# Optimization experiments

Hardware: AMD Instinct MI355X
Metric: run time of the kernel (lower is better)

## Reference

```python
import jax, jax.numpy as jnp
import numpy as np

B, S, D, H, L, C = 64, 2048, 64, 256, 2, 8  # batch, seq, input, hidden, layers, classes


def setup_inputs() -> dict:
    key = jax.random.key(0)
    ks = jax.random.split(key, 12)
    k = 1.0 / np.sqrt(H)  # torch LSTM/Linear init scale
    u = lambda kk, shape: jax.random.uniform(kk, shape, jnp.float32, -k, k)
    x = jax.random.normal(ks[0], (B, S, D), jnp.float32)
    lengths = jax.random.randint(ks[1], (B,), 1, S + 1).astype(jnp.int32)
    return {
        "x": x,
        "lengths": lengths,
        "Wih0": u(ks[2], (4 * H, D)),
        "Whh0": u(ks[3], (4 * H, H)),
        "bih0": u(ks[4], (4 * H,)),
        "bhh0": u(ks[5], (4 * H,)),
        "Wih1": u(ks[6], (4 * H, H)),
        "Whh1": u(ks[7], (4 * H, H)),
        "bih1": u(ks[8], (4 * H,)),
        "bhh1": u(ks[9], (4 * H,)),
        "Wfc": u(ks[10], (C, H)),
        "bfc": u(ks[11], (C,)),
    }


def _lstm_layer(x, Wih, Whh, bih, bhh):
    # x: [B,S,Din] -> h-sequence [B,S,H]; torch gate order i,f,g,o
    pre = jnp.einsum('bsd,gd->bsg', x, Wih) + bih + bhh  # [B,S,4H]
    Hh = Whh.shape[1]
    bsz = x.shape[0]

    def step(carry, p_t):
        h, c = carry
        gates = p_t + h @ Whh.T  # [B,4H]
        i, f, g, o = jnp.split(gates, 4, axis=-1)
        i = jax.nn.sigmoid(i)
        f = jax.nn.sigmoid(f)
        g = jnp.tanh(g)
        o = jax.nn.sigmoid(o)
        c = f * c + i * g
        h = o * jnp.tanh(c)
        return (h, c), h

    init = (jnp.zeros((bsz, Hh), x.dtype), jnp.zeros((bsz, Hh), x.dtype))
    _, hs = jax.lax.scan(step, init, jnp.swapaxes(pre, 0, 1))  # [S,B,H]
    return jnp.swapaxes(hs, 0, 1)


def reference(x, lengths, Wih0, Whh0, bih0, bhh0, Wih1, Whh1, bih1, bhh1, Wfc, bfc):
    h1 = _lstm_layer(x, Wih0, Whh0, bih0, bhh0)   # [B,S,H]
    h2 = _lstm_layer(h1, Wih1, Whh1, bih1, bhh1)  # [B,S,H]
    # pad_packed_sequence zeros outputs beyond each sequence's length
    valid = (jnp.arange(S)[None, :] < lengths[:, None])[..., None]  # [B,S,1]
    h2 = jnp.where(valid, h2, 0.0)
    emissions = jnp.einsum('bsh,ch->bsc', h2, Wfc) + bfc  # [B,S,C]
    return emissions
```

## Files before the change

kernel.cpp:

```cpp
#include <hip/hip_runtime.h>
#include <hip/hip_bf16.h>

#define BATCH 64
#define SEQ   2048
#define DIN   64
#define HID   256
#define G4H   1024
#define NCLS  8

__device__ __forceinline__ float sigm(float x)  { return 1.0f / (1.0f + __expf(-x)); }
__device__ __forceinline__ float tanh_f(float x){ return 1.0f - 2.0f / (__expf(2.0f * x) + 1.0f); }

__global__ void init_out_kernel(float* __restrict__ out, const float* __restrict__ bfc) {
    int idx = blockIdx.x * blockDim.x + threadIdx.x;
    if (idx < BATCH * SEQ * NCLS) out[idx] = bfc[idx & 7];
}

__global__ __launch_bounds__(1024) void lstm_l0_kernel(
    const float* __restrict__ x,    const float* __restrict__ Wih0,
    const float* __restrict__ Whh0, const float* __restrict__ bih0,
    const float* __restrict__ bhh0, float* __restrict__ hist,
    const float* __restrict__ h1s_in, float* __restrict__ h1s_out,
    float* __restrict__ c1s, int* __restrict__ flagsA, int t0, int t1)
{
    const int bx  = blockIdx.x;
    const int b   = bx & 63;
    const int mem = bx >> 6;
    const int tid = threadIdx.x;
    const int p   = tid >> 8;
    const int r   = tid & 255;
    const int row = (r >> 6) * 256 + mem * 64 + (r & 63);

    float w[80];
#pragma unroll
    for (int q = 0; q < 80; ++q) {
        int col = p * 80 + q;
        w[q] = (col < DIN) ? Wih0[row * DIN + col] : Whh0[row * HID + (col - DIN)];
    }
    float biasv = 0.f;
    if (tid < 256) {
        int row2 = (tid >> 6) * 256 + mem * 64 + (tid & 63);
        biasv = bih0[row2] + bhh0[row2];
    }
    float creg = 0.f;
    if (tid < 64) creg = c1s[b * HID + mem * 64 + tid];

    __shared__ __align__(16) float v[320];
    __shared__ float pbuf[1024];
    __shared__ float act[256];

    for (int t = t0; t < t1; ++t) {
        if (t > t0 && tid < 4) {
            while (__hip_atomic_load(&flagsA[b * 4 + tid], __ATOMIC_ACQUIRE,
                                     __HIP_MEMORY_SCOPE_AGENT) < t) {}
        }
        __syncthreads();
        if (tid < 64) {
            v[tid] = x[((size_t)b * SEQ + t) * DIN + tid];
        } else if (tid < 320) {
            int j = tid - 64;
            v[tid] = (t == t0)
                ? h1s_in[b * HID + j]
                : __hip_atomic_load(&hist[((size_t)(t - 1 - t0) * BATCH + b) * HID + j],
                                    __ATOMIC_RELAXED, __HIP_MEMORY_SCOPE_AGENT);
        }
        __syncthreads();

        float a0 = 0.f, a1 = 0.f, a2 = 0.f, a3 = 0.f;
#pragma unroll
        for (int qq = 0; qq < 20; ++qq) {
            float4 vv = *(const float4*)&v[p * 80 + qq * 4];
            a0 = fmaf(w[qq * 4 + 0], vv.x, a0);
            a1 = fmaf(w[qq * 4 + 1], vv.y, a1);
            a2 = fmaf(w[qq * 4 + 2], vv.z, a2);
            a3 = fmaf(w[qq * 4 + 3], vv.w, a3);
        }
        pbuf[tid] = (a0 + a1) + (a2 + a3);
        __syncthreads();

        if (tid < 256) {
            float s = pbuf[tid] + pbuf[256 + tid] + pbuf[512 + tid] + pbuf[768 + tid] + biasv;
            act[tid] = ((tid >> 6) == 2) ? tanh_f(s) : sigm(s);
        }
        __syncthreads();

        if (tid < 64) {
            float iv = act[tid], fv = act[64 + tid], gv = act[128 + tid], ov = act[192 + tid];
            creg = fv * creg + iv * gv;
            float h = ov * tanh_f(creg);
            __hip_atomic_store(&hist[((size_t)(t - t0) * BATCH + b) * HID + mem * 64 + tid],
                               h, __ATOMIC_RELAXED, __HIP_MEMORY_SCOPE_AGENT);
            if (t == t1 - 1) {
                h1s_out[b * HID + mem * 64 + tid] = h;
                c1s[b * HID + mem * 64 + tid]     = creg;
            }
        }
        __syncthreads();
        if (tid == 0) {
            __hip_atomic_store(&flagsA[b * 4 + mem], t + 1, __ATOMIC_RELEASE,
                               __HIP_MEMORY_SCOPE_AGENT);
        }
    }
}

__global__ __launch_bounds__(1024) void lstm_l1_kernel(
    const float* __restrict__ hist, const float* __restrict__ Wih1,
    const float* __restrict__ Whh1, const float* __restrict__ bih1,
    const float* __restrict__ bhh1, const float* __restrict__ Wfc,
    const int* __restrict__ lengths, float* __restrict__ out,
    const float* __restrict__ h2s_in, float* __restrict__ h2s_out,
    float* __restrict__ c2s, float* __restrict__ xbuf,
    int* __restrict__ flagsB, int t0, int t1)
{
    const int bx  = blockIdx.x;
    const int bp  = bx & 31;
    const int mem = bx >> 5;
    const int tid = threadIdx.x;
    const int p   = tid >> 7;
    const int r   = tid & 127;
    const int row = (r >> 5) * 256 + mem * 32 + (r & 31);

    float w[64];
#pragma unroll
    for (int q = 0; q < 64; ++q) {
        int col = p * 64 + q;
        w[q] = (col < HID) ? Wih1[row * HID + col] : Whh1[row * HID + (col - HID)];
    }
    float biasv = 0.f;
    if (tid < 256) {
        int rr = tid & 127;
        int row2 = (rr >> 5) * 256 + mem * 32 + (rr & 31);
        biasv = bih1[row2] + bhh1[row2];
    }
    float creg = 0.f;
    if (tid < 64) {
        int n = tid >> 5, j2 = tid & 31;
        creg = c2s[(bp * 2 + n) * HID + mem * 32 + j2];
    }
    float wfc_r = 0.f; int mylen = 0;
    if (tid < 512) {
        int n = tid >> 8, c = (tid >> 5) & 7, j3 = tid & 31;
        wfc_r = Wfc[c * HID + mem * 32 + j3];
        mylen = lengths[bp * 2 + n];
    }

    __shared__ __align__(16) float vbuf[1024];
    __shared__ float pbuf[2048];
    __shared__ float act[256];
    __shared__ float hloc[64];

    for (int t = t0; t < t1; ++t) {
        if (t > t0 && tid < 8) {
            while (__hip_atomic_load(&flagsB[bp * 8 + tid], __ATOMIC_ACQUIRE,
                                     __HIP_MEMORY_SCOPE_AGENT) < t) {}
        }
        __syncthreads();
        if (tid < 512) {
            int n = tid >> 8, j = tid & 255;
            float hv = (t == t0)
                ? h2s_in[(bp * 2 + n) * HID + j]
                : __hip_atomic_load(&xbuf[((bp * 2 + n) * 2 + ((t - 1) & 1)) * HID + j],
                                    __ATOMIC_RELAXED, __HIP_MEMORY_SCOPE_AGENT);
            vbuf[n * 512 + HID + j] = hv;
        } else {
            int k = tid - 512;
            int n = k >> 8, j = k & 255;
            vbuf[n * 512 + j] = hist[((size_t)(t - t0) * BATCH + (bp * 2 + n)) * HID + j];
        }
        __syncthreads();

        float acc0 = 0.f, acc1 = 0.f;
#pragma unroll
        for (int qq = 0; qq < 16; ++qq) {
            float4 va = *(const float4*)&vbuf[p * 64 + qq * 4];
            acc0 = fmaf(w[qq * 4 + 0], va.x, acc0);
            acc0 = fmaf(w[qq * 4 + 1], va.y, acc0);
            acc0 = fmaf(w[qq * 4 + 2], va.z, acc0);
            acc0 = fmaf(w[qq * 4 + 3], va.w, acc0);
            float4 vb = *(const float4*)&vbuf[512 + p * 64 + qq * 4];
            acc1 = fmaf(w[qq * 4 + 0], vb.x, acc1);
            acc1 = fmaf(w[qq * 4 + 1], vb.y, acc1);
            acc1 = fmaf(w[qq * 4 + 2], vb.z, acc1);
            acc1 = fmaf(w[qq * 4 + 3], vb.w, acc1);
        }
        pbuf[p * 128 + r]        = acc0;
        pbuf[1024 + p * 128 + r] = acc1;
        __syncthreads();

        if (tid < 256) {
            int n = tid >> 7, rr = tid & 127;
            float s = biasv;
#pragma unroll
            for (int q = 0; q < 8; ++q) s += pbuf[n * 1024 + q * 128 + rr];
            act[n * 128 + rr] = ((rr >> 5) == 2) ? tanh_f(s) : sigm(s);
        }
        __syncthreads();

        if (tid < 64) {
            int n = tid >> 5, j2 = tid & 31;
            float iv = act[n * 128 + j2],      fv = act[n * 128 + 32 + j2];
            float gv = act[n * 128 + 64 + j2], ov = act[n * 128 + 96 + j2];
            creg = fv * creg + iv * gv;
            float h = ov * tanh_f(creg);
            hloc[tid] = h;
            __hip_atomic_store(&xbuf[((bp * 2 + n) * 2 + (t & 1)) * HID + mem * 32 + j2],
                               h, __ATOMIC_RELAXED, __HIP_MEMORY_SCOPE_AGENT);
            if (t == t1 - 1) {
                h2s_out[(bp * 2 + n) * HID + mem * 32 + j2] = h;
                c2s[(bp * 2 + n) * HID + mem * 32 + j2]     = creg;
            }
        }
        __syncthreads();
        if (tid == 0) {
            __hip_atomic_store(&flagsB[bp * 8 + mem], t + 1, __ATOMIC_RELEASE,
                               __HIP_MEMORY_SCOPE_AGENT);
        }
        if (tid < 512) {
            int n = tid >> 8, c = (tid >> 5) & 7, j3 = tid & 31;
            float val = (t < mylen) ? hloc[n * 32 + j3] * wfc_r : 0.f;
            val += __shfl_xor(val, 1);
            val += __shfl_xor(val, 2);
            val += __shfl_xor(val, 4);
            val += __shfl_xor(val, 8);
            val += __shfl_xor(val, 16);
            if (j3 == 0)
                atomicAdd(&out[((size_t)(bp * 2 + n) * SEQ + t) * NCLS + c], val);
        }
    }
}

extern "C" void kernel_launch(void* const* d_in, const int* in_sizes, int n_in,
                              void* d_out, int out_size, void* d_ws, size_t ws_size,
                              hipStream_t stream) {
    (void)in_sizes; (void)n_in; (void)out_size;
    const float* x     = (const float*)d_in[0];
    const int*   lens  = (const int*)  d_in[1];
    const float* Wih0  = (const float*)d_in[2];
    const float* Whh0  = (const float*)d_in[3];
    const float* bih0  = (const float*)d_in[4];
    const float* bhh0  = (const float*)d_in[5];
    const float* Wih1  = (const float*)d_in[6];
    const float* Whh1  = (const float*)d_in[7];
    const float* bih1  = (const float*)d_in[8];
    const float* bhh1  = (const float*)d_in[9];
    const float* Wfc   = (const float*)d_in[10];
    const float* bfc   = (const float*)d_in[11];
    float* out = (float*)d_out;
    char*  ws  = (char*)d_ws;

    int*   flagsA = (int*)(ws + 0);
    int*   flagsB = (int*)(ws + 1024);
    float* h1sA   = (float*)(ws + 2048);
    float* h1sB   = (float*)(ws + 2048 + 1 * 65536);
    float* c1s    = (float*)(ws + 2048 + 2 * 65536);
    float* h2sA   = (float*)(ws + 2048 + 3 * 65536);
    float* h2sB   = (float*)(ws + 2048 + 4 * 65536);
    float* c2s    = (float*)(ws + 2048 + 5 * 65536);
    float* xbuf   = (float*)(ws + 2048 + 6 * 65536);
    size_t hist_off = 2048 + 6 * 65536 + 131072;
    hist_off = (hist_off + 255) & ~(size_t)255;
    float* hist = (float*)(ws + hist_off);

    const size_t step_bytes = (size_t)BATCH * HID * 4;
    if (ws_size < hist_off + step_bytes) return;
    long avail = (long)(ws_size - hist_off);
    int Tc = (int)(avail / (long)step_bytes);
    if (Tc > SEQ) Tc = SEQ;
    if (Tc < 1)  Tc = 1;

    hipMemsetAsync(ws, 0, hist_off, stream);
    init_out_kernel<<<(BATCH * SEQ * NCLS + 255) / 256, 256, 0, stream>>>(out, bfc);

    int flip = 0;
    for (int t0 = 0; t0 < SEQ; t0 += Tc) {
        int t1 = t0 + Tc; if (t1 > SEQ) t1 = SEQ;
        float* h1in  = flip ? h1sB : h1sA;
        float* h1out = flip ? h1sA : h1sB;
        float* h2in  = flip ? h2sB : h2sA;
        float* h2out = flip ? h2sA : h2sB;
        lstm_l0_kernel<<<256, 1024, 0, stream>>>(x, Wih0, Whh0, bih0, bhh0, hist,
                                                 h1in, h1out, c1s, flagsA, t0, t1);
        lstm_l1_kernel<<<256, 1024, 0, stream>>>(hist, Wih1, Whh1, bih1, bhh1, Wfc,
                                                 lens, out, h2in, h2out, c2s, xbuf,
                                                 flagsB, t0, t1);
        flip ^= 1;
    }
}
```

Measured before the change: 19.92 ms.

## Regroup LSTM work per block and run whole sequence in single launches

Layer 0 now has each block handle two batch rows and a 32-unit slice, so the 256-block grid uses 8 member blocks per batch pair. Layer 1 has each block handle four batch rows and a 16-unit slice, with 16-way flag synchronisation. The output projection is now computed from the previous step's hidden state inside the step's existing barriers and stored directly instead of through atomicAdd. Time chunking is removed and a full-sequence history buffer is required, which drops the saved h/c state between chunks but needs a larger workspace. The layer-1 loop also removes one barrier per step, and the sync groups get wider, which may raise spin-wait cost.

```diff
diff --git a/kernel.cpp b/kernel.cpp
--- a/kernel.cpp
+++ b/kernel.cpp
@@ -5,7 +5,6 @@
 #define SEQ   2048
 #define DIN   64
 #define HID   256
-#define G4H   1024
 #define NCLS  8
 
 __device__ __forceinline__ float sigm(float x)  { return 1.0f / (1.0f + __expf(-x)); }
@@ -16,175 +15,79 @@
     if (idx < BATCH * SEQ * NCLS) out[idx] = bfc[idx & 7];
 }
 
-__global__ __launch_bounds__(1024) void lstm_l0_kernel(
+__global__ void lstm_l0_kernel(
     const float* __restrict__ x,    const float* __restrict__ Wih0,
     const float* __restrict__ Whh0, const float* __restrict__ bih0,
     const float* __restrict__ bhh0, float* __restrict__ hist,
-    const float* __restrict__ h1s_in, float* __restrict__ h1s_out,
-    float* __restrict__ c1s, int* __restrict__ flagsA, int t0, int t1)
+    int* __restrict__ flagsA)
 {
-    const int bx  = blockIdx.x;
-    const int b   = bx & 63;
-    const int mem = bx >> 6;
-    const int tid = threadIdx.x;
-    const int p   = tid >> 8;
-    const int r   = tid & 255;
-    const int row = (r >> 6) * 256 + mem * 64 + (r & 63);
-
-    float w[80];
-#pragma unroll
-    for (int q = 0; q < 80; ++q) {
-        int col = p * 80 + q;
-        w[q] = (col < DIN) ? Wih0[row * DIN + col] : Whh0[row * HID + (col - DIN)];
-    }
-    float biasv = 0.f;
-    if (tid < 256) {
-        int row2 = (tid >> 6) * 256 + mem * 64 + (tid & 63);
-        biasv = bih0[row2] + bhh0[row2];
-    }
-    float creg = 0.f;
-    if (tid < 64) creg = c1s[b * HID + mem * 64 + tid];
-
-    __shared__ __align__(16) float v[320];
-    __shared__ float pbuf[1024];
-    __shared__ float act[256];
-
-    for (int t = t0; t < t1; ++t) {
-        if (t > t0 && tid < 4) {
-            while (__hip_atomic_load(&flagsA[b * 4 + tid], __ATOMIC_ACQUIRE,
-                                     __HIP_MEMORY_SCOPE_AGENT) < t) {}
-        }
-        __syncthreads();
-        if (tid < 64) {
-            v[tid] = x[((size_t)b * SEQ + t) * DIN + tid];
-        } else if (tid < 320) {
-            int j = tid - 64;
-            v[tid] = (t == t0)
-                ? h1s_in[b * HID + j]
-                : __hip_atomic_load(&hist[((size_t)(t - 1 - t0) * BATCH + b) * HID + j],
-                                    __ATOMIC_RELAXED, __HIP_MEMORY_SCOPE_AGENT);
-        }
-        __syncthreads();
-
-        float a0 = 0.f, a1 = 0.f, a2 = 0.f, a3 = 0.f;
-#pragma unroll
-        for (int qq = 0; qq < 20; ++qq) {
-            float4 vv = *(const float4*)&v[p * 80 + qq * 4];
-            a0 = fmaf(w[qq * 4 + 0], vv.x, a0);
-            a1 = fmaf(w[qq * 4 + 1], vv.y, a1);
-            a2 = fmaf(w[qq * 4 + 2], vv.z, a2);
-            a3 = fmaf(w[qq * 4 + 3], vv.w, a3);
-        }
-        pbuf[tid] = (a0 + a1) + (a2 + a3);
-        __syncthreads();
-
-        if (tid < 256) {
-            float s = pbuf[tid] + pbuf[256 + tid] + pbuf[512 + tid] + pbuf[768 + tid] + biasv;
-            act[tid] = ((tid >> 6) == 2) ? tanh_f(s) : sigm(s);
-        }
-        __syncthreads();
-
-        if (tid < 64) {
-            float iv = act[tid], fv = act[64 + tid], gv = act[128 + tid], ov = act[192 + tid];
-            creg = fv * creg + iv * gv;
-            float h = ov * tanh_f(creg);
-            __hip_atomic_store(&hist[((size_t)(t - t0) * BATCH + b) * HID + mem * 64 + tid],
-                               h, __ATOMIC_RELAXED, __HIP_MEMORY_SCOPE_AGENT);
-            if (t == t1 - 1) {
-                h1s_out[b * HID + mem * 64 + tid] = h;
-                c1s[b * HID + mem * 64 + tid]     = creg;
-            }
-        }
-        __syncthreads();
-        if (tid == 0) {
-            __hip_atomic_store(&flagsA[b * 4 + mem], t + 1, __ATOMIC_RELEASE,
-                               __HIP_MEMORY_SCOPE_AGENT);
-        }
-    }
-}
-
-__global__ __launch_bounds__(1024) void lstm_l1_kernel(
-    const float* __restrict__ hist, const float* __restrict__ Wih1,
-    const float* __restrict__ Whh1, const float* __restrict__ bih1,
-    const float* __restrict__ bhh1, const float* __restrict__ Wfc,
-    const int* __restrict__ lengths, float* __restrict__ out,
-    const float* __restrict__ h2s_in, float* __restrict__ h2s_out,
-    float* __restrict__ c2s, float* __restrict__ xbuf,
-    int* __restrict__ flagsB, int t0, int t1)
-{
-    const int bx  = blockIdx.x;
-    const int bp  = bx & 31;
-    const int mem = bx >> 5;
+    const int P   = blockIdx.x & 31;
+    const int mem = blockIdx.x >> 5;
     const int tid = threadIdx.x;
     const int p   = tid >> 7;
     const int r   = tid & 127;
     const int row = (r >> 5) * 256 + mem * 32 + (r & 31);
 
-    float w[64];
-#pragma unroll
-    for (int q = 0; q < 64; ++q) {
-        int col = p * 64 + q;
-        w[q] = (col < HID) ? Wih1[row * HID + col] : Whh1[row * HID + (col - HID)];
-    }
+    float w[40];
+#pragma unroll
+    for (int q = 0; q < 40; ++q) {
+        int col = p * 40 + q;
+        w[q] = (col < DIN) ? Wih0[row * DIN + col] : Whh0[row * HID + (col - DIN)];
+    }
+#pragma unroll
+    for (int q = 0; q < 40; ++q) asm volatile("" : "+v"(w[q]));
+
     float biasv = 0.f;
     if (tid < 256) {
         int rr = tid & 127;
         int row2 = (rr >> 5) * 256 + mem * 32 + (rr & 31);
-        biasv = bih1[row2] + bhh1[row2];
-    }
+        biasv = bih0[row2] + bhh0[row2];
+    }
+    asm volatile("" : "+v"(biasv));
     float creg = 0.f;
-    if (tid < 64) {
-        int n = tid >> 5, j2 = tid & 31;
-        creg = c2s[(bp * 2 + n) * HID + mem * 32 + j2];
-    }
-    float wfc_r = 0.f; int mylen = 0;
-    if (tid < 512) {
-        int n = tid >> 8, c = (tid >> 5) & 7, j3 = tid & 31;
-        wfc_r = Wfc[c * HID + mem * 32 + j3];
-        mylen = lengths[bp * 2 + n];
-    }
-
-    __shared__ __align__(16) float vbuf[1024];
+
+    __shared__ __align__(16) float v[640];
     __shared__ float pbuf[2048];
     __shared__ float act[256];
-    __shared__ float hloc[64];
-
-    for (int t = t0; t < t1; ++t) {
-        if (t > t0 && tid < 8) {
-            while (__hip_atomic_load(&flagsB[bp * 8 + tid], __ATOMIC_ACQUIRE,
+
+    for (int t = 0; t < SEQ; ++t) {
+        if (t > 0 && tid < 8) {
+            while (__hip_atomic_load(&flagsA[P * 8 + tid], __ATOMIC_ACQUIRE,
                                      __HIP_MEMORY_SCOPE_AGENT) < t) {}
         }
         __syncthreads();
-        if (tid < 512) {
-            int n = tid >> 8, j = tid & 255;
-            float hv = (t == t0)
-                ? h2s_in[(bp * 2 + n) * HID + j]
-                : __hip_atomic_load(&xbuf[((bp * 2 + n) * 2 + ((t - 1) & 1)) * HID + j],
-                                    __ATOMIC_RELAXED, __HIP_MEMORY_SCOPE_AGENT);
-            vbuf[n * 512 + HID + j] = hv;
-        } else {
-            int k = tid - 512;
-            int n = k >> 8, j = k & 255;
-            vbuf[n * 512 + j] = hist[((size_t)(t - t0) * BATCH + (bp * 2 + n)) * HID + j];
-        }
-        __syncthreads();
-
-        float acc0 = 0.f, acc1 = 0.f;
-#pragma unroll
-        for (int qq = 0; qq < 16; ++qq) {
-            float4 va = *(const float4*)&vbuf[p * 64 + qq * 4];
-            acc0 = fmaf(w[qq * 4 + 0], va.x, acc0);
-            acc0 = fmaf(w[qq * 4 + 1], va.y, acc0);
-            acc0 = fmaf(w[qq * 4 + 2], va.z, acc0);
-            acc0 = fmaf(w[qq * 4 + 3], va.w, acc0);
-            float4 vb = *(const float4*)&vbuf[512 + p * 64 + qq * 4];
-            acc1 = fmaf(w[qq * 4 + 0], vb.x, acc1);
-            acc1 = fmaf(w[qq * 4 + 1], vb.y, acc1);
-            acc1 = fmaf(w[qq * 4 + 2], vb.z, acc1);
-            acc1 = fmaf(w[qq * 4 + 3], vb.w, acc1);
-        }
-        pbuf[p * 128 + r]        = acc0;
-        pbuf[1024 + p * 128 + r] = acc1;
+        if (tid < 640) {
+            int n = (tid >= 320) ? 1 : 0;
+            int j = tid - n * 320;
+            int b = 2 * P + n;
+            float val;
+            if (j < DIN) {
+                val = x[((size_t)b * SEQ + t) * DIN + j];
+            } else {
+                val = (t == 0) ? 0.f
+                    : __hip_atomic_load(&hist[((size_t)(t - 1) * BATCH + b) * HID + (j - DIN)],
+                                        __ATOMIC_RELAXED, __HIP_MEMORY_SCOPE_AGENT);
+            }
+            v[n * 320 + j] = val;
+        }
+        __syncthreads();
+
+        float a0 = 0.f, a1 = 0.f;
+#pragma unroll
+        for (int qq = 0; qq < 10; ++qq) {
+            float4 va = *(const float4*)&v[p * 40 + qq * 4];
+            a0 = fmaf(w[qq * 4 + 0], va.x, a0);
+            a0 = fmaf(w[qq * 4 + 1], va.y, a0);
+            a0 = fmaf(w[qq * 4 + 2], va.z, a0);
+            a0 = fmaf(w[qq * 4 + 3], va.w, a0);
+            float4 vb = *(const float4*)&v[320 + p * 40 + qq * 4];
+            a1 = fmaf(w[qq * 4 + 0], vb.x, a1);
+            a1 = fmaf(w[qq * 4 + 1], vb.y, a1);
+            a1 = fmaf(w[qq * 4 + 2], vb.z, a1);
+            a1 = fmaf(w[qq * 4 + 3], vb.w, a1);
+        }
+        pbuf[p * 128 + r]        = a0;
+        pbuf[1024 + p * 128 + r] = a1;
         __syncthreads();
 
         if (tid < 256) {
@@ -197,35 +100,169 @@
         __syncthreads();
 
         if (tid < 64) {
-            int n = tid >> 5, j2 = tid & 31;
-            float iv = act[n * 128 + j2],      fv = act[n * 128 + 32 + j2];
-            float gv = act[n * 128 + 64 + j2], ov = act[n * 128 + 96 + j2];
+            int n = tid >> 5, k = tid & 31, b = 2 * P + n;
+            float iv = act[n * 128 + k],      fv = act[n * 128 + 32 + k];
+            float gv = act[n * 128 + 64 + k], ov = act[n * 128 + 96 + k];
             creg = fv * creg + iv * gv;
             float h = ov * tanh_f(creg);
-            hloc[tid] = h;
-            __hip_atomic_store(&xbuf[((bp * 2 + n) * 2 + (t & 1)) * HID + mem * 32 + j2],
+            __hip_atomic_store(&hist[((size_t)t * BATCH + b) * HID + mem * 32 + k],
                                h, __ATOMIC_RELAXED, __HIP_MEMORY_SCOPE_AGENT);
-            if (t == t1 - 1) {
-                h2s_out[(bp * 2 + n) * HID + mem * 32 + j2] = h;
-                c2s[(bp * 2 + n) * HID + mem * 32 + j2]     = creg;
-            }
-        }
-        __syncthreads();
+        }
         if (tid == 0) {
-            __hip_atomic_store(&flagsB[bp * 8 + mem], t + 1, __ATOMIC_RELEASE,
+            __hip_atomic_store(&flagsA[P * 8 + mem], t + 1, __ATOMIC_RELEASE,
                                __HIP_MEMORY_SCOPE_AGENT);
         }
-        if (tid < 512) {
-            int n = tid >> 8, c = (tid >> 5) & 7, j3 = tid & 31;
-            float val = (t < mylen) ? hloc[n * 32 + j3] * wfc_r : 0.f;
-            val += __shfl_xor(val, 1);
-            val += __shfl_xor(val, 2);
-            val += __shfl_xor(val, 4);
-            val += __shfl_xor(val, 8);
-            val += __shfl_xor(val, 16);
-            if (j3 == 0)
-                atomicAdd(&out[((size_t)(bp * 2 + n) * SEQ + t) * NCLS + c], val);
-        }
+    }
+}
+
+__global__ void lstm_l1_kernel(
+    const float* __restrict__ hist, const float* __restrict__ Wih1,
+    const float* __restrict__ Whh1, const float* __restrict__ bih1,
+    const float* __restrict__ bhh1, const float* __restrict__ Wfc,
+    const float* __restrict__ bfc,  const int* __restrict__ lengths,
+    float* __restrict__ out, float* __restrict__ xbuf, int* __restrict__ flagsB)
+{
+    const int g   = blockIdx.x & 15;
+    const int mem = blockIdx.x >> 4;
+    const int tid = threadIdx.x;
+    const int p   = tid >> 6;
+    const int r   = tid & 63;
+    const int row = (r >> 4) * 256 + mem * 16 + (r & 15);
+
+    float w[32];
+#pragma unroll
+    for (int q = 0; q < 32; ++q) {
+        int col = p * 32 + q;
+        w[q] = (col < HID) ? Wih1[row * HID + col] : Whh1[row * HID + (col - HID)];
+    }
+#pragma unroll
+    for (int q = 0; q < 32; ++q) asm volatile("" : "+v"(w[q]));
+
+    float biasv = 0.f;
+    if (tid < 256) {
+        int rr = tid & 63;
+        int row2 = (rr >> 4) * 256 + mem * 16 + (rr & 15);
+        biasv = bih1[row2] + bhh1[row2];
+    }
+    asm volatile("" : "+v"(biasv));
+    float creg = 0.f;
+
+    const int nf = mem & 3;
+    const int c0 = (mem >> 2) * 2;
+    float wfc = 0.f;
+    if (tid < 512) wfc = Wfc[(c0 + (tid >> 8)) * HID + (tid & 255)];
+    asm volatile("" : "+v"(wfc));
+    const int  lenb = lengths[4 * g + nf];
+    float bfcv = (tid < 2) ? bfc[c0 + tid] : 0.f;
+
+    __shared__ __align__(16) float vbuf[2048];
+    __shared__ float pbuf[4096];
+    __shared__ float act[256];
+    __shared__ float fcred[8];
+
+    for (int t = 0; t < SEQ; ++t) {
+        if (t > 0 && tid < 16) {
+            while (__hip_atomic_load(&flagsB[g * 16 + tid], __ATOMIC_ACQUIRE,
+                                     __HIP_MEMORY_SCOPE_AGENT) < t) {}
+        }
+        __syncthreads();
+        {
+            int n = tid >> 8, j = tid & 255, b = 4 * g + n;
+            vbuf[n * 512 + j] = hist[((size_t)t * BATCH + b) * HID + j];
+            float hv = (t == 0) ? 0.f
+                : __hip_atomic_load(&xbuf[((size_t)b * 2 + ((t - 1) & 1)) * HID + j],
+                                    __ATOMIC_RELAXED, __HIP_MEMORY_SCOPE_AGENT);
+            vbuf[n * 512 + HID + j] = hv;
+        }
+        __syncthreads();
+
+        float a0 = 0.f, a1 = 0.f, a2 = 0.f, a3 = 0.f;
+#pragma unroll
+        for (int qq = 0; qq < 8; ++qq) {
+            float4 v0 = *(const float4*)&vbuf[p * 32 + qq * 4];
+            a0 = fmaf(w[qq * 4 + 0], v0.x, a0); a0 = fmaf(w[qq * 4 + 1], v0.y, a0);
+            a0 = fmaf(w[qq * 4 + 2], v0.z, a0); a0 = fmaf(w[qq * 4 + 3], v0.w, a0);
+            float4 v1 = *(const float4*)&vbuf[512 + p * 32 + qq * 4];
+            a1 = fmaf(w[qq * 4 + 0], v1.x, a1); a1 = fmaf(w[qq * 4 + 1], v1.y, a1);
+            a1 = fmaf(w[qq * 4 + 2], v1.z, a1); a1 = fmaf(w[qq * 4 + 3], v1.w, a1);
+            float4 v2 = *(const float4*)&vbuf[1024 + p * 32 + qq * 4];
+            a2 = fmaf(w[qq * 4 + 0], v2.x, a2); a2 = fmaf(w[qq * 4 + 1], v2.y, a2);
+            a2 = fmaf(w[qq * 4 + 2], v2.z, a2); a2 = fmaf(w[qq * 4 + 3], v2.w, a2);
+            float4 v3 = *(const float4*)&vbuf[1536 + p * 32 + qq * 4];
+            a3 = fmaf(w[qq * 4 + 0], v3.x, a3); a3 = fmaf(w[qq * 4 + 1], v3.y, a3);
+            a3 = fmaf(w[qq * 4 + 2], v3.z, a3); a3 = fmaf(w[qq * 4 + 3], v3.w, a3);
+        }
+        pbuf[p * 64 + r]        = a0;
+        pbuf[1024 + p * 64 + r] = a1;
+        pbuf[2048 + p * 64 + r] = a2;
+        pbuf[3072 + p * 64 + r] = a3;
+
+        float fval = 0.f;
+        if (t > 0 && tid < 512) {
+            fval = vbuf[nf * 512 + HID + (tid & 255)] * wfc;
+            fval += __shfl_xor(fval, 1);
+            fval += __shfl_xor(fval, 2);
+            fval += __shfl_xor(fval, 4);
+            fval += __shfl_xor(fval, 8);
+            fval += __shfl_xor(fval, 16);
+            fval += __shfl_xor(fval, 32);
+            if ((tid & 63) == 0) fcred[tid >> 6] = fval;
+        }
+        __syncthreads();
+
+        if (tid < 256) {
+            int n = tid >> 6, rw = tid & 63;
+            float s = biasv;
+#pragma unroll
+            for (int q = 0; q < 16; ++q) s += pbuf[n * 1024 + q * 64 + rw];
+            act[n * 64 + rw] = ((rw >> 4) == 2) ? tanh_f(s) : sigm(s);
+        }
+        if (t > 0 && tid < 2 && (t - 1) < lenb) {
+            float s2 = fcred[tid * 4 + 0] + fcred[tid * 4 + 1]
+                     + fcred[tid * 4 + 2] + fcred[tid * 4 + 3];
+            out[((size_t)(4 * g + nf) * SEQ + (t - 1)) * NCLS + c0 + tid] = bfcv + s2;
+        }
+        __syncthreads();
+
+        if (tid < 64) {
+            int n = tid >> 4, k = tid & 15, b = 4 * g + n;
+            float iv = act[n * 64 + k],      fv = act[n * 64 + 16 + k];
+            float gv = act[n * 64 + 32 + k], ov = act[n * 64 + 48 + k];
+            creg = fv * creg + iv * gv;
+            float h = ov * tanh_f(creg);
+            __hip_atomic_store(&xbuf[((size_t)b * 2 + (t & 1)) * HID + mem * 16 + k],
+                               h, __ATOMIC_RELAXED, __HIP_MEMORY_SCOPE_AGENT);
+        }
+        if (tid == 0) {
+            __hip_atomic_store(&flagsB[g * 16 + mem], t + 1, __ATOMIC_RELEASE,
+                               __HIP_MEMORY_SCOPE_AGENT);
+        }
+    }
+
+    if (tid < 16) {
+        while (__hip_atomic_load(&flagsB[g * 16 + tid], __ATOMIC_ACQUIRE,
+                                 __HIP_MEMORY_SCOPE_AGENT) < SEQ) {}
+    }
+    __syncthreads();
+    float fval = 0.f;
+    if (tid < 512) {
+        int b = 4 * g + nf;
+        float hv = __hip_atomic_load(&xbuf[((size_t)b * 2 + ((SEQ - 1) & 1)) * HID + (tid & 255)],
+                                     __ATOMIC_RELAXED, __HIP_MEMORY_SCOPE_AGENT);
+        fval = hv * wfc;
+        fval += __shfl_xor(fval, 1);
+        fval += __shfl_xor(fval, 2);
+        fval += __shfl_xor(fval, 4);
+        fval += __shfl_xor(fval, 8);
+        fval += __shfl_xor(fval, 16);
+        fval += __shfl_xor(fval, 32);
+        if ((tid & 63) == 0) fcred[tid >> 6] = fval;
+    }
+    __syncthreads();
+    if (tid < 2 && (SEQ - 1) < lenb) {
+        float s2 = fcred[tid * 4 + 0] + fcred[tid * 4 + 1]
+                 + fcred[tid * 4 + 2] + fcred[tid * 4 + 3];
+        out[((size_t)(4 * g + nf) * SEQ + (SEQ - 1)) * NCLS + c0 + tid] = bfcv + s2;
     }
 }
 
@@ -248,41 +285,17 @@
     float* out = (float*)d_out;
     char*  ws  = (char*)d_ws;
 
-    int*   flagsA = (int*)(ws + 0);
+    int*   flagsA = (int*)(ws);
     int*   flagsB = (int*)(ws + 1024);
-    float* h1sA   = (float*)(ws + 2048);
-    float* h1sB   = (float*)(ws + 2048 + 1 * 65536);
-    float* c1s    = (float*)(ws + 2048 + 2 * 65536);
-    float* h2sA   = (float*)(ws + 2048 + 3 * 65536);
-    float* h2sB   = (float*)(ws + 2048 + 4 * 65536);
-    float* c2s    = (float*)(ws + 2048 + 5 * 65536);
-    float* xbuf   = (float*)(ws + 2048 + 6 * 65536);
-    size_t hist_off = 2048 + 6 * 65536 + 131072;
-    hist_off = (hist_off + 255) & ~(size_t)255;
+    float* xbuf   = (float*)(ws + 2048);
+    const size_t hist_off = 2048 + (size_t)BATCH * 2 * HID * 4;
     float* hist = (float*)(ws + hist_off);
-
-    const size_t step_bytes = (size_t)BATCH * HID * 4;
-    if (ws_size < hist_off + step_bytes) return;
-    long avail = (long)(ws_size - hist_off);
-    int Tc = (int)(avail / (long)step_bytes);
-    if (Tc > SEQ) Tc = SEQ;
-    if (Tc < 1)  Tc = 1;
+    const size_t need = hist_off + (size_t)SEQ * BATCH * HID * 4;
+    if (ws_size < need) return;
 
     hipMemsetAsync(ws, 0, hist_off, stream);
     init_out_kernel<<<(BATCH * SEQ * NCLS + 255) / 256, 256, 0, stream>>>(out, bfc);
-
-    int flip = 0;
-    for (int t0 = 0; t0 < SEQ; t0 += Tc) {
-        int t1 = t0 + Tc; if (t1 > SEQ) t1 = SEQ;
-        float* h1in  = flip ? h1sB : h1sA;
-        float* h1out = flip ? h1sA : h1sB;
-        float* h2in  = flip ? h2sB : h2sA;
-        float* h2out = flip ? h2sA : h2sB;
-        lstm_l0_kernel<<<256, 1024, 0, stream>>>(x, Wih0, Whh0, bih0, bhh0, hist,
-                                                 h1in, h1out, c1s, flagsA, t0, t1);
-        lstm_l1_kernel<<<256, 1024, 0, stream>>>(hist, Wih1, Whh1, bih1, bhh1, Wfc,
-                                                 lens, out, h2in, h2out, c2s, xbuf,
-                                                 flagsB, t0, t1);
-        flip ^= 1;
-    }
+    lstm_l0_kernel<<<256, 1024, 0, stream>>>(x, Wih0, Whh0, bih0, bhh0, hist, flagsA);
+    lstm_l1_kernel<<<256, 1024, 0, stream>>>(hist, Wih1, Whh1, bih1, bhh1, Wfc, bfc,
+                                             lens, out, xbuf, flagsB);
 }
```

Measured after the change: 24.18 ms. +21.4%, slower.
